# Kernel tuning notes

Measured on AMD Instinct MI355X. Metric: run time of the kernel, lower is better.

Reference implementation:

```python
import jax, jax.numpy as jnp
import numpy as np

ALPHA = 1.0
BETA = 0.25
NUM_EMBEDS = 8192
EMBED_DIM = 512
B, T = 32, 256


def setup_inputs() -> dict:
    key = jax.random.key(0)
    k1, k2 = jax.random.split(key)
    z_e = jax.random.normal(k1, (B, EMBED_DIM, T), dtype=jnp.float32)
    codebook = jax.random.normal(k2, (NUM_EMBEDS, EMBED_DIM), dtype=jnp.float32)
    return {"z_e": z_e, "codebook": codebook}


def reference(z_e, codebook):
    # z_e: (b, d, t) -> (b, t, d)
    z = jnp.transpose(z_e, (0, 2, 1))
    b, t, d = z.shape
    flat = z.reshape(-1, d)  # (N, d), N = b*t

    # squared euclidean distances to every codebook vector: (N, K)
    dists = (
        jnp.sum(flat * flat, axis=1, keepdims=True)
        + jnp.sum(codebook * codebook, axis=1)
        - 2.0 * flat @ codebook.T
    )
    idx = jnp.argmin(dists, axis=1)  # (N,)

    # codebook lookup (equivalent to one-hot @ codebook)
    z_q = codebook[idx].reshape(b, t, d)

    # commitment loss (codebook is EMA-updated, so only e_latent term)
    e_latent_loss = jnp.mean((jax.lax.stop_gradient(z_q) - z) ** 2)
    vq_loss = ALPHA * BETA * e_latent_loss

    # straight-through estimator
    z_q_st = z + jax.lax.stop_gradient(z_q - z)
    z_q_out = jnp.transpose(z_q_st, (0, 2, 1))  # back to (b, d, t)

    # perplexity from mean one-hot assignment probabilities
    counts = jnp.zeros((codebook.shape[0],), dtype=jnp.float32).at[idx].add(1.0)
    avg_probs = counts / flat.shape[0]
    perplexity = jnp.exp(-jnp.sum(avg_probs * jnp.log(avg_probs + 1e-10)))

    return z_q_out, vq_loss, perplexity
```

## Files before the change

### kernel.cpp

```cpp
#include <hip/hip_runtime.h>
#include <stdint.h>

typedef _Float16 half8 __attribute__((ext_vector_type(8)));
typedef float floatx16 __attribute__((ext_vector_type(16)));
typedef unsigned long long u64;

#define ALPHA_ 1.0f
#define BETA_ 0.25f
#define NUM_EMBEDS 8192
#define EMBED_DIM 512
#define B_ 32
#define T_ 256
#define N_TOK 8192
#define THR_GAP 2e-3f


typedef __attribute__((address_space(1))) const void ga_void;
typedef __attribute__((address_space(3))) void ls_void;
__device__ __forceinline__ void gl_lds16(const void* g, void* l) {
    __builtin_amdgcn_global_load_lds((ga_void*)g, (ls_void*)l, 16, 0, 0);
}

__device__ __forceinline__ uint32_t mono(float s) {
    uint32_t u = __float_as_uint(s);
    return (u & 0x80000000u) ? ~u : (u | 0x80000000u);
}
__device__ __forceinline__ float unmono(uint32_t v) {
    return __uint_as_float((v & 0x80000000u) ? (v ^ 0x80000000u) : ~v);
}

__global__ void pack_cb_kernel(const float* __restrict__ cb, _Float16* __restrict__ ci,
                               float* __restrict__ cnorm) {
    int row = blockIdx.x * 4 + (threadIdx.x >> 6);
    int lane = threadIdx.x & 63;
    const float* src = cb + (size_t)row * EMBED_DIM + lane * 8;
    float4 v0 = *(const float4*)src;
    float4 v1 = *(const float4*)(src + 4);
    float x[8] = {v0.x, v0.y, v0.z, v0.w, v1.x, v1.y, v1.z, v1.w};
    half8 hh, mm;
    float s = 0.f;
#pragma unroll
    for (int j = 0; j < 8; ++j) {
        s += x[j] * x[j];
        _Float16 hv = (_Float16)x[j];
        hh[j] = hv;
        mm[j] = (_Float16)((x[j] - (float)hv) * 2048.0f);
    }
    _Float16* dst = ci + (size_t)row * 1024 + lane * 16;
    *(half8*)dst = hh;
    *(half8*)(dst + 8) = mm;
#pragma unroll
    for (int d = 32; d; d >>= 1) s += __shfl_xor(s, d, 64);
    if (lane == 0) cnorm[row] = s;
}

__global__ void pack_z_kernel(const float* __restrict__ z, _Float16* __restrict__ zi) {
    int tid = threadIdx.x;
    int lane = tid & 63, ds = tid >> 6;
    int b = blockIdx.x >> 2;
    int t = ((blockIdx.x & 3) << 6) + lane;
    size_t n = (size_t)b * T_ + t;
    for (int g = 0; g < 16; ++g) {
        int d0 = g * 32 + ds * 8;
        const float* src = z + ((size_t)b * EMBED_DIM + d0) * T_ + t;
        half8 hh, mm;
#pragma unroll
        for (int j = 0; j < 8; ++j) {
            float x = -2.0f * src[(size_t)j * T_];
            _Float16 hv = (_Float16)x;
            hh[j] = hv;
            mm[j] = (_Float16)((x - (float)hv) * 2048.0f);
        }
        _Float16* dst = zi + n * 1024 + (size_t)(g * 4 + ds) * 16;
        *(half8*)dst = hh;
        *(half8*)(dst + 8) = mm;
    }
}

#define MFMA16(a, b, c) __builtin_amdgcn_mfma_f32_32x32x16_f16(a, b, c, 0, 0, 0)

__global__ __launch_bounds__(256, 2) void argmin_kernel(
    const _Float16* __restrict__ cb_i, const _Float16* __restrict__ zt_i,
    const float* __restrict__ cnorm, u64* __restrict__ slot_m1,
    _Float16* __restrict__ slot_d) {
    __shared__ _Float16 As[2][8192];
    __shared__ _Float16 Bs[2][8192];
    __shared__ u64 sK[128];
    __shared__ float sV1[128], sV2[128];
    const int tid = threadIdx.x;
    const int l = tid & 63;
    const int wv = tid >> 6;
    const int l31 = l & 31;
    const int hf = l >> 5;
    const int wp = wv >> 1, wq = wv & 1;
    const int n0 = blockIdx.x * 128;
    const int c0 = blockIdx.y * 128;

    const bool isA = wv < 2;
    const _Float16* gsrc = isA ? cb_i : zt_i;
    const int rbase = (isA ? c0 : n0) + ((wv & 1) << 6);
    const int srow = l >> 3;
    const int sseg = (l & 7) ^ srow;
    const size_t lanefix = (size_t)(rbase + srow) * 1024 + sseg * 8;

    floatx16 acc1[2][2], acc2[2][2];
#pragma unroll
    for (int a = 0; a < 2; ++a)
#pragma unroll
        for (int b = 0; b < 2; ++b)
#pragma unroll
            for (int r = 0; r < 16; ++r) { acc1[a][b][r] = 0.f; acc2[a][b][r] = 0.f; }

    auto stage = [&](int p, int s) {
        const _Float16* gs = gsrc + lanefix + (size_t)s * 64;
        _Float16* lb = (isA ? As[p] : Bs[p]) + ((wv & 1) << 12);
#pragma unroll
        for (int j = 0; j < 8; ++j)
            gl_lds16(gs + (size_t)j * 8192, lb + j * 512);
    };

    stage(0, 0);
    __syncthreads();
    for (int s = 0; s < 16; ++s) {
        const int p = s & 1;
        if (s < 15) stage(p ^ 1, s + 1);
        const _Float16* Ab = As[p] + (wp * 64 + l31) * 64;
        const _Float16* Bb = Bs[p] + (wq * 64 + l31) * 64;
        const int rs = l31 & 7;
#pragma unroll
        for (int kk = 0; kk < 2; ++kk) {
            const int j = kk * 2 + hf;
            const int ph = ((2 * j) ^ rs) * 8;
            const int pm = ((2 * j + 1) ^ rs) * 8;
            half8 Ah0 = *(const half8*)(Ab + ph), Am0 = *(const half8*)(Ab + pm);
            half8 Ah1 = *(const half8*)(Ab + 2048 + ph), Am1 = *(const half8*)(Ab + 2048 + pm);
            half8 Bh0 = *(const half8*)(Bb + ph), Bm0 = *(const half8*)(Bb + pm);
            half8 Bh1 = *(const half8*)(Bb + 2048 + ph), Bm1 = *(const half8*)(Bb + 2048 + pm);
            acc1[0][0] = MFMA16(Ah0, Bh0, acc1[0][0]);
            acc2[0][0] = MFMA16(Ah0, Bm0, acc2[0][0]);
            acc2[0][0] = MFMA16(Am0, Bh0, acc2[0][0]);
            acc1[0][1] = MFMA16(Ah0, Bh1, acc1[0][1]);
            acc2[0][1] = MFMA16(Ah0, Bm1, acc2[0][1]);
            acc2[0][1] = MFMA16(Am0, Bh1, acc2[0][1]);
            acc1[1][0] = MFMA16(Ah1, Bh0, acc1[1][0]);
            acc2[1][0] = MFMA16(Ah1, Bm0, acc2[1][0]);
            acc2[1][0] = MFMA16(Am1, Bh0, acc2[1][0]);
            acc1[1][1] = MFMA16(Ah1, Bh1, acc1[1][1]);
            acc2[1][1] = MFMA16(Ah1, Bm1, acc2[1][1]);
            acc2[1][1] = MFMA16(Am1, Bh1, acc2[1][1]);
        }
        __syncthreads();
    }

    u64 km[2]; float kv1[2], kv2[2];
#pragma unroll
    for (int qi = 0; qi < 2; ++qi) {
        u64 m1k = ~0ULL;
        float m1v = 3.4e38f, m2 = 3.4e38f;
#pragma unroll
        for (int ti = 0; ti < 2; ++ti)
#pragma unroll
            for (int g = 0; g < 4; ++g) {
                const int cb4 = c0 + wp * 64 + ti * 32 + g * 8 + hf * 4;
                float4 cn = *(const float4*)(cnorm + cb4);
                const floatx16& A1 = acc1[ti][qi];
                const floatx16& A2 = acc2[ti][qi];
                float sv[4] = {cn.x + A1[g * 4 + 0] + A2[g * 4 + 0] * (1.0f / 2048.0f),
                               cn.y + A1[g * 4 + 1] + A2[g * 4 + 1] * (1.0f / 2048.0f),
                               cn.z + A1[g * 4 + 2] + A2[g * 4 + 2] * (1.0f / 2048.0f),
                               cn.w + A1[g * 4 + 3] + A2[g * 4 + 3] * (1.0f / 2048.0f)};
#pragma unroll
                for (int q = 0; q < 4; ++q) {
                    u64 key = ((u64)mono(sv[q]) << 32) | (uint32_t)(cb4 + q);
                    if (key < m1k) { m2 = m1v; m1v = sv[q]; m1k = key; }
                    else m2 = fminf(m2, sv[q]);
                }
            }
        u64 ok = __shfl_xor(m1k, 32, 64);
        float ov = __shfl_xor(m1v, 32, 64);
        float om2 = __shfl_xor(m2, 32, 64);
        if (ok < m1k) { m2 = fminf(fminf(m2, om2), m1v); m1v = ov; m1k = ok; }
        else m2 = fminf(fminf(m2, om2), ov);
        km[qi] = m1k; kv1[qi] = m1v; kv2[qi] = m2;
    }
    if (wp == 1 && hf == 0) {
#pragma unroll
        for (int qi = 0; qi < 2; ++qi) {
            int idx = wq * 64 + qi * 32 + l31;
            sK[idx] = km[qi]; sV1[idx] = kv1[qi]; sV2[idx] = kv2[qi];
        }
    }
    __syncthreads();
    if (wp == 0 && hf == 0) {
#pragma unroll
        for (int qi = 0; qi < 2; ++qi) {
            int idx = wq * 64 + qi * 32 + l31;
            u64 m1k = km[qi]; float m1v = kv1[qi], m2 = kv2[qi];
            u64 ok = sK[idx]; float ov = sV1[idx], om2 = sV2[idx];
            if (ok < m1k) { m2 = fminf(fminf(m2, om2), m1v); m1v = ov; m1k = ok; }
            else m2 = fminf(fminf(m2, om2), ov);
            int tok = n0 + idx;
            slot_m1[((size_t)blockIdx.y << 13) + tok] = m1k;
            slot_d[((size_t)blockIdx.y << 13) + tok] = (_Float16)(m2 - m1v);
        }
    }
}

__global__ void combine_kernel(const u64* __restrict__ slot_m1, const _Float16* __restrict__ slot_d,
                               u64* __restrict__ wexact, int* __restrict__ worklist,
                               int* __restrict__ nflag) {
    int tok = blockIdx.x * 256 + threadIdx.x;
    u64 g1 = ~0ULL;
    float g1v = 3.4e38f, g2 = 3.4e38f;
    for (int c = 0; c < 64; ++c) {
        u64 k = slot_m1[((size_t)c << 13) + tok];
        float kv = unmono((uint32_t)(k >> 32));
        float v2 = kv + (float)slot_d[((size_t)c << 13) + tok];
        if (k < g1) { g2 = fminf(g2, g1v); g1 = k; g1v = kv; }
        else g2 = fminf(g2, kv);
        g2 = fminf(g2, v2);
    }
    if (g2 - g1v > THR_GAP) wexact[tok] = g1;
    else { int i = atomicAdd(nflag, 1); if (i < 8192) worklist[i] = tok; }
}

__global__ void fallback_kernel(const float* __restrict__ z, const float* __restrict__ cb,
                                const float* __restrict__ cnorm,
                                const int* __restrict__ worklist, const int* __restrict__ nflag,
                                u64* __restrict__ wexact) {
    int n = *nflag;
    if (n > 8192) n = 8192;
    const int l = threadIdx.x & 63, wv = threadIdx.x >> 6;
    const int cbase = blockIdx.x * 128;
    for (int fi = blockIdx.y; fi < n; fi += gridDim.y) {
        int tok = worklist[fi];
        int b = tok >> 8, t = tok & 255;
        const float* zp = z + ((size_t)b * EMBED_DIM) * T_ + t;
        float zr[8];
#pragma unroll
        for (int j = 0; j < 8; ++j) zr[j] = zp[(size_t)(l * 8 + j) * T_];
        u64 m1 = ~0ULL;
        for (int j = 0; j < 32; ++j) {
            int c = cbase + wv + j * 4;
            const float* cp = cb + (size_t)c * EMBED_DIM + l * 8;
            float4 a = *(const float4*)cp, bb = *(const float4*)(cp + 4);
            float dot = zr[0] * a.x + zr[1] * a.y + zr[2] * a.z + zr[3] * a.w +
                        zr[4] * bb.x + zr[5] * bb.y + zr[6] * bb.z + zr[7] * bb.w;
#pragma unroll
            for (int m = 32; m; m >>= 1) dot += __shfl_xor(dot, m, 64);
            if (l == 0) {
                float s = cnorm[c] - 2.0f * dot;
                u64 key = ((u64)mono(s) << 32) | (uint32_t)c;
                if (key < m1) m1 = key;
            }
        }
        if (l == 0) atomicMin(&wexact[tok], m1);
    }
}

__global__ void gather_kernel(const float* __restrict__ z, const float* __restrict__ cb,
                              const u64* __restrict__ wexact,
                              float* __restrict__ out, int* __restrict__ counts,
                              float* __restrict__ sse_acc) {
    __shared__ unsigned int sIdx[64];
    __shared__ float red[4];
    const int tid = threadIdx.x;
    const int n0 = blockIdx.x * 64;
    const int b = n0 >> 8;
    const int t0 = n0 & 255;
    if (tid < 64) {
        unsigned int idx = (unsigned int)(wexact[n0 + tid] & 0xffffffffULL);
        sIdx[tid] = idx;
        atomicAdd(&counts[idx], 1);
    }
    __syncthreads();
    const int w = tid >> 6;
    const int lane = tid & 63;
    const float* crow = cb + (size_t)sIdx[lane] * EMBED_DIM;
    const size_t base = ((size_t)b * EMBED_DIM) * T_ + (size_t)(t0 + lane);
    float sse = 0.f;
    for (int d = w; d < EMBED_DIM; d += 4) {
        float v = crow[d];
        size_t o = base + (size_t)d * T_;
        float diff = v - z[o];
        out[o] = v;
        sse += diff * diff;
    }
    for (int m = 32; m; m >>= 1) sse += __shfl_xor(sse, m, 64);
    if (lane == 0) red[w] = sse;
    __syncthreads();
    if (tid == 0) atomicAdd(sse_acc, red[0] + red[1] + red[2] + red[3]);
}

__global__ void finalize_kernel(const int* __restrict__ counts,
                                const float* __restrict__ sse_acc,
                                float* __restrict__ out) {
    __shared__ float red[4];
    const int tid = threadIdx.x;
    float e = 0.f;
    for (int k = tid; k < NUM_EMBEDS; k += 256) {
        float p = (float)counts[k] * (1.0f / (float)N_TOK);
        e += p * logf(p + 1e-10f);
    }
    for (int m = 32; m; m >>= 1) e += __shfl_xor(e, m, 64);
    if ((tid & 63) == 0) red[tid >> 6] = e;
    __syncthreads();
    if (tid == 0) {
        float ent = red[0] + red[1] + red[2] + red[3];
        size_t off = (size_t)B_ * EMBED_DIM * T_;
        out[off + 0] = (ALPHA_ * BETA_) * sse_acc[0] / (float)((size_t)N_TOK * EMBED_DIM);
        out[off + 1] = expf(-ent);
    }
}

extern "C" void kernel_launch(void* const* d_in, const int* in_sizes, int n_in,
                              void* d_out, int out_size, void* d_ws, size_t ws_size,
                              hipStream_t stream) {
    const float* z = (const float*)d_in[0];
    const float* cb = (const float*)d_in[1];
    float* out = (float*)d_out;
    char* ws = (char*)d_ws;
    u64* wexact = (u64*)ws;
    float* cnorm = (float*)(ws + 65536);
    int* counts = (int*)(ws + 98304);
    float* sse = (float*)(ws + 131072);
    int* nflag = (int*)(ws + 131076);
    int* worklist = (int*)(ws + 131080);
    u64* slot_m1 = (u64*)(ws + (1ull << 20));
    _Float16* slot_d = (_Float16*)(ws + (5ull << 20));
    _Float16* cb_i = (_Float16*)(ws + (6ull << 20));
    _Float16* zt_i = (_Float16*)(ws + (22ull << 20));

    hipMemsetAsync(wexact, 0xFF, NUM_EMBEDS * sizeof(u64), stream);
    hipMemsetAsync(counts, 0, NUM_EMBEDS * sizeof(int) + 8, stream);

    pack_cb_kernel<<<NUM_EMBEDS / 4, 256, 0, stream>>>(cb, cb_i, cnorm);
    pack_z_kernel<<<N_TOK / 64, 256, 0, stream>>>(z, zt_i);
    argmin_kernel<<<dim3(N_TOK / 128, NUM_EMBEDS / 128), 256, 0, stream>>>(cb_i, zt_i, cnorm, slot_m1, slot_d);
    combine_kernel<<<N_TOK / 256, 256, 0, stream>>>(slot_m1, slot_d, wexact, worklist, nflag);
    fallback_kernel<<<dim3(64, 16), 256, 0, stream>>>(z, cb, cnorm, worklist, nflag, wexact);
    gather_kernel<<<N_TOK / 64, 256, 0, stream>>>(z, cb, wexact, out, counts, sse);
    finalize_kernel<<<1, 256, 0, stream>>>(counts, sse, out);
}
```

Baseline: 363.3 us.

## Retile split-fp16 argmin GEMM, fuse pack/init kernels, pack slot data

The argmin GEMM now uses 256-token by 128-code tiles with a single combined accumulator per output tile instead of separate hi and correction accumulators. It also uses a K step of 32 over 32 stages and a new swizzled LDS layout, with the next stage's loads issued after the fragment reads. The two pack kernels and both memsets are merged into one launch. The per-slot min key and gap are packed into a single u64, so combine reads one array. The residual is stored unscaled, so its precision drops, and THR_GAP is raised to compensate, which may send more tokens to the exact fallback.

```diff
diff --git a/kernel.cpp b/kernel.cpp
--- a/kernel.cpp
+++ b/kernel.cpp
@@ -12,7 +12,7 @@
 #define B_ 32
 #define T_ 256
 #define N_TOK 8192
-#define THR_GAP 2e-3f
+#define THR_GAP 0.01f
 
 
 typedef __attribute__((address_space(1))) const void ga_void;
@@ -29,51 +29,62 @@
     return __uint_as_float((v & 0x80000000u) ? (v ^ 0x80000000u) : ~v);
 }
 
-__global__ void pack_cb_kernel(const float* __restrict__ cb, _Float16* __restrict__ ci,
-                               float* __restrict__ cnorm) {
-    int row = blockIdx.x * 4 + (threadIdx.x >> 6);
-    int lane = threadIdx.x & 63;
-    const float* src = cb + (size_t)row * EMBED_DIM + lane * 8;
-    float4 v0 = *(const float4*)src;
-    float4 v1 = *(const float4*)(src + 4);
-    float x[8] = {v0.x, v0.y, v0.z, v0.w, v1.x, v1.y, v1.z, v1.w};
-    half8 hh, mm;
-    float s = 0.f;
-#pragma unroll
-    for (int j = 0; j < 8; ++j) {
-        s += x[j] * x[j];
-        _Float16 hv = (_Float16)x[j];
-        hh[j] = hv;
-        mm[j] = (_Float16)((x[j] - (float)hv) * 2048.0f);
-    }
-    _Float16* dst = ci + (size_t)row * 1024 + lane * 16;
-    *(half8*)dst = hh;
-    *(half8*)(dst + 8) = mm;
-#pragma unroll
-    for (int d = 32; d; d >>= 1) s += __shfl_xor(s, d, 64);
-    if (lane == 0) cnorm[row] = s;
-}
-
-__global__ void pack_z_kernel(const float* __restrict__ z, _Float16* __restrict__ zi) {
-    int tid = threadIdx.x;
-    int lane = tid & 63, ds = tid >> 6;
-    int b = blockIdx.x >> 2;
-    int t = ((blockIdx.x & 3) << 6) + lane;
-    size_t n = (size_t)b * T_ + t;
-    for (int g = 0; g < 16; ++g) {
-        int d0 = g * 32 + ds * 8;
-        const float* src = z + ((size_t)b * EMBED_DIM + d0) * T_ + t;
+__global__ void pack_kernel(const float* __restrict__ cb, const float* __restrict__ z,
+                            _Float16* __restrict__ cb_i, _Float16* __restrict__ zt_i,
+                            float* __restrict__ cnorm, u64* __restrict__ wexact,
+                            int* __restrict__ counts, float* __restrict__ sse,
+                            int* __restrict__ nflag) {
+    const int bx = blockIdx.x;
+    const int tid = threadIdx.x;
+    if (bx < 2048) {
+        int row = bx * 4 + (tid >> 6);
+        int lane = tid & 63;
+        const float* src = cb + (size_t)row * EMBED_DIM + lane * 8;
+        float4 v0 = *(const float4*)src;
+        float4 v1 = *(const float4*)(src + 4);
+        float x[8] = {v0.x, v0.y, v0.z, v0.w, v1.x, v1.y, v1.z, v1.w};
         half8 hh, mm;
+        float s = 0.f;
 #pragma unroll
         for (int j = 0; j < 8; ++j) {
-            float x = -2.0f * src[(size_t)j * T_];
-            _Float16 hv = (_Float16)x;
+            s += x[j] * x[j];
+            _Float16 hv = (_Float16)x[j];
             hh[j] = hv;
-            mm[j] = (_Float16)((x - (float)hv) * 2048.0f);
-        }
-        _Float16* dst = zi + n * 1024 + (size_t)(g * 4 + ds) * 16;
+            mm[j] = (_Float16)(x[j] - (float)hv);
+        }
+        _Float16* dst = cb_i + (size_t)row * 1024 + (lane >> 1) * 32 + (lane & 1) * 8;
         *(half8*)dst = hh;
-        *(half8*)(dst + 8) = mm;
+        *(half8*)(dst + 16) = mm;
+#pragma unroll
+        for (int d = 32; d; d >>= 1) s += __shfl_xor(s, d, 64);
+        if (lane == 0) cnorm[row] = s;
+    } else if (bx < 2176) {
+        int bz = bx - 2048;
+        int lane = tid & 63, ds = tid >> 6;
+        int b = bz >> 2;
+        int t = ((bz & 3) << 6) + lane;
+        size_t n = (size_t)b * T_ + t;
+        for (int g = 0; g < 16; ++g) {
+            int d0 = g * 32 + ds * 8;
+            const float* src = z + ((size_t)b * EMBED_DIM + d0) * T_ + t;
+            half8 hh, mm;
+#pragma unroll
+            for (int j = 0; j < 8; ++j) {
+                float x = -2.0f * src[(size_t)j * T_];
+                _Float16 hv = (_Float16)x;
+                hh[j] = hv;
+                mm[j] = (_Float16)(x - (float)hv);
+            }
+            int gg = g * 4 + ds;
+            _Float16* dst = zt_i + n * 1024 + (gg >> 1) * 32 + (gg & 1) * 8;
+            *(half8*)dst = hh;
+            *(half8*)(dst + 16) = mm;
+        }
+    } else {
+        int i = bx - 2176;
+        wexact[i * 256 + tid] = ~0ULL;
+        counts[i * 256 + tid] = 0;
+        if (i == 0 && tid == 0) { *sse = 0.f; *nflag = 0; }
     }
 }
 
@@ -81,94 +92,113 @@
 
 __global__ __launch_bounds__(256, 2) void argmin_kernel(
     const _Float16* __restrict__ cb_i, const _Float16* __restrict__ zt_i,
-    const float* __restrict__ cnorm, u64* __restrict__ slot_m1,
-    _Float16* __restrict__ slot_d) {
-    __shared__ _Float16 As[2][8192];
-    __shared__ _Float16 Bs[2][8192];
-    __shared__ u64 sK[128];
-    __shared__ float sV1[128], sV2[128];
+    const float* __restrict__ cnorm, u64* __restrict__ slot) {
+    __shared__ _Float16 smem[24576];
+    __shared__ u64 sK[256];
+    __shared__ float sV1[256], sV2[256];
     const int tid = threadIdx.x;
     const int l = tid & 63;
     const int wv = tid >> 6;
     const int l31 = l & 31;
     const int hf = l >> 5;
     const int wp = wv >> 1, wq = wv & 1;
-    const int n0 = blockIdx.x * 128;
+    const int n0 = blockIdx.x * 256;
     const int c0 = blockIdx.y * 128;
 
-    const bool isA = wv < 2;
-    const _Float16* gsrc = isA ? cb_i : zt_i;
-    const int rbase = (isA ? c0 : n0) + ((wv & 1) << 6);
-    const int srow = l >> 3;
-    const int sseg = (l & 7) ^ srow;
-    const size_t lanefix = (size_t)(rbase + srow) * 1024 + sseg * 8;
-
-    floatx16 acc1[2][2], acc2[2][2];
-#pragma unroll
-    for (int a = 0; a < 2; ++a)
-#pragma unroll
-        for (int b = 0; b < 2; ++b)
-#pragma unroll
-            for (int r = 0; r < 16; ++r) { acc1[a][b][r] = 0.f; acc2[a][b][r] = 0.f; }
-
-    auto stage = [&](int p, int s) {
-        const _Float16* gs = gsrc + lanefix + (size_t)s * 64;
-        _Float16* lb = (isA ? As[p] : Bs[p]) + ((wv & 1) << 12);
-#pragma unroll
-        for (int j = 0; j < 8; ++j)
-            gl_lds16(gs + (size_t)j * 8192, lb + j * 512);
+    const _Float16* gptr[6];
+    int lofs[6], bmul[6];
+#pragma unroll
+    for (int j = 0; j < 6; ++j) {
+        int id = wv * 6 + j;
+        if (id < 8) {
+            int rp = id * 4 + (l >> 4);
+            int lid = (l & 15) ^ (rp & 15);
+            gptr[j] = cb_i + (size_t)(c0 + (lid >> 2) * 32 + rp) * 1024 + (lid & 3) * 8;
+            lofs[j] = id * 512 + l * 8;
+            bmul[j] = 4096;
+        } else {
+            int bid = id - 8;
+            int rp = bid * 4 + (l >> 4);
+            int lid = (l & 15) ^ (rp & 15);
+            gptr[j] = zt_i + (size_t)(n0 + (lid >> 2) * 64 + rp) * 1024 + (lid & 3) * 8;
+            lofs[j] = 8192 + bid * 512 + l * 8;
+            bmul[j] = 8192;
+        }
+    }
+    auto stagefull = [&](int buf, int ss) {
+        const int ga = ss * 32;
+#pragma unroll
+        for (int j = 0; j < 6; ++j)
+            gl_lds16(gptr[j] + ga, smem + lofs[j] + buf * bmul[j]);
     };
 
-    stage(0, 0);
-    __syncthreads();
-    for (int s = 0; s < 16; ++s) {
-        const int p = s & 1;
-        if (s < 15) stage(p ^ 1, s + 1);
-        const _Float16* Ab = As[p] + (wp * 64 + l31) * 64;
-        const _Float16* Bb = Bs[p] + (wq * 64 + l31) * 64;
-        const int rs = l31 & 7;
-#pragma unroll
-        for (int kk = 0; kk < 2; ++kk) {
-            const int j = kk * 2 + hf;
-            const int ph = ((2 * j) ^ rs) * 8;
-            const int pm = ((2 * j + 1) ^ rs) * 8;
-            half8 Ah0 = *(const half8*)(Ab + ph), Am0 = *(const half8*)(Ab + pm);
-            half8 Ah1 = *(const half8*)(Ab + 2048 + ph), Am1 = *(const half8*)(Ab + 2048 + pm);
-            half8 Bh0 = *(const half8*)(Bb + ph), Bm0 = *(const half8*)(Bb + pm);
-            half8 Bh1 = *(const half8*)(Bb + 2048 + ph), Bm1 = *(const half8*)(Bb + 2048 + pm);
-            acc1[0][0] = MFMA16(Ah0, Bh0, acc1[0][0]);
-            acc2[0][0] = MFMA16(Ah0, Bm0, acc2[0][0]);
-            acc2[0][0] = MFMA16(Am0, Bh0, acc2[0][0]);
-            acc1[0][1] = MFMA16(Ah0, Bh1, acc1[0][1]);
-            acc2[0][1] = MFMA16(Ah0, Bm1, acc2[0][1]);
-            acc2[0][1] = MFMA16(Am0, Bh1, acc2[0][1]);
-            acc1[1][0] = MFMA16(Ah1, Bh0, acc1[1][0]);
-            acc2[1][0] = MFMA16(Ah1, Bm0, acc2[1][0]);
-            acc2[1][0] = MFMA16(Am1, Bh0, acc2[1][0]);
-            acc1[1][1] = MFMA16(Ah1, Bh1, acc1[1][1]);
-            acc2[1][1] = MFMA16(Ah1, Bm1, acc2[1][1]);
-            acc2[1][1] = MFMA16(Am1, Bh1, acc2[1][1]);
-        }
+    int aoff[2][2], boff[4][2];
+#pragma unroll
+    for (int pi = 0; pi < 2; ++pi)
+#pragma unroll
+        for (int p = 0; p < 2; ++p) {
+            int lid = (wp * 2 + pi) * 4 + p * 2 + hf;
+            aoff[pi][p] = l31 * 128 + (lid ^ (l31 & 15)) * 8;
+        }
+#pragma unroll
+    for (int qi = 0; qi < 4; ++qi)
+#pragma unroll
+        for (int p = 0; p < 2; ++p) {
+            int lid = (wq * 2 + (qi >> 1)) * 4 + p * 2 + hf;
+            boff[qi][p] = 8192 + ((qi & 1) * 32 + l31) * 128 + (lid ^ (l31 & 15)) * 8;
+        }
+
+    floatx16 acc[2][4];
+#pragma unroll
+    for (int pi = 0; pi < 2; ++pi)
+#pragma unroll
+        for (int qi = 0; qi < 4; ++qi)
+#pragma unroll
+            for (int r = 0; r < 16; ++r) acc[pi][qi][r] = 0.f;
+
+    stagefull(0, 0);
+    __syncthreads();
+    for (int ss = 0; ss < 32; ++ss) {
+        const int buf = ss & 1;
+        const int ab = buf * 4096, bb = buf * 8192;
+        half8 Ah[2], Am[2], Bh[4], Bm[4];
+#pragma unroll
+        for (int pi = 0; pi < 2; ++pi) {
+            Ah[pi] = *(const half8*)(smem + aoff[pi][0] + ab);
+            Am[pi] = *(const half8*)(smem + aoff[pi][1] + ab);
+        }
+#pragma unroll
+        for (int qi = 0; qi < 4; ++qi) {
+            Bh[qi] = *(const half8*)(smem + boff[qi][0] + bb);
+            Bm[qi] = *(const half8*)(smem + boff[qi][1] + bb);
+        }
+        if (ss < 31) stagefull(buf ^ 1, ss + 1);
+#pragma unroll
+        for (int pi = 0; pi < 2; ++pi)
+#pragma unroll
+            for (int qi = 0; qi < 4; ++qi) {
+                acc[pi][qi] = MFMA16(Ah[pi], Bh[qi], acc[pi][qi]);
+                acc[pi][qi] = MFMA16(Am[pi], Bh[qi], acc[pi][qi]);
+                acc[pi][qi] = MFMA16(Ah[pi], Bm[qi], acc[pi][qi]);
+            }
         __syncthreads();
     }
 
-    u64 km[2]; float kv1[2], kv2[2];
-#pragma unroll
-    for (int qi = 0; qi < 2; ++qi) {
+    u64 qk[4];
+    float qv1[4], qv2[4];
+#pragma unroll
+    for (int qi = 0; qi < 4; ++qi) {
         u64 m1k = ~0ULL;
         float m1v = 3.4e38f, m2 = 3.4e38f;
 #pragma unroll
-        for (int ti = 0; ti < 2; ++ti)
+        for (int pi = 0; pi < 2; ++pi)
 #pragma unroll
             for (int g = 0; g < 4; ++g) {
-                const int cb4 = c0 + wp * 64 + ti * 32 + g * 8 + hf * 4;
+                const int cb4 = c0 + wp * 64 + pi * 32 + g * 8 + hf * 4;
                 float4 cn = *(const float4*)(cnorm + cb4);
-                const floatx16& A1 = acc1[ti][qi];
-                const floatx16& A2 = acc2[ti][qi];
-                float sv[4] = {cn.x + A1[g * 4 + 0] + A2[g * 4 + 0] * (1.0f / 2048.0f),
-                               cn.y + A1[g * 4 + 1] + A2[g * 4 + 1] * (1.0f / 2048.0f),
-                               cn.z + A1[g * 4 + 2] + A2[g * 4 + 2] * (1.0f / 2048.0f),
-                               cn.w + A1[g * 4 + 3] + A2[g * 4 + 3] * (1.0f / 2048.0f)};
+                const floatx16& A = acc[pi][qi];
+                float sv[4] = {cn.x + A[g * 4 + 0], cn.y + A[g * 4 + 1],
+                               cn.z + A[g * 4 + 2], cn.w + A[g * 4 + 3]};
 #pragma unroll
                 for (int q = 0; q < 4; ++q) {
                     u64 key = ((u64)mono(sv[q]) << 32) | (uint32_t)(cb4 + q);
@@ -181,46 +211,47 @@
         float om2 = __shfl_xor(m2, 32, 64);
         if (ok < m1k) { m2 = fminf(fminf(m2, om2), m1v); m1v = ov; m1k = ok; }
         else m2 = fminf(fminf(m2, om2), ov);
-        km[qi] = m1k; kv1[qi] = m1v; kv2[qi] = m2;
+        qk[qi] = m1k; qv1[qi] = m1v; qv2[qi] = m2;
     }
     if (wp == 1 && hf == 0) {
 #pragma unroll
-        for (int qi = 0; qi < 2; ++qi) {
-            int idx = wq * 64 + qi * 32 + l31;
-            sK[idx] = km[qi]; sV1[idx] = kv1[qi]; sV2[idx] = kv2[qi];
+        for (int qi = 0; qi < 4; ++qi) {
+            const int tl = wq * 128 + qi * 32 + l31;
+            sK[tl] = qk[qi]; sV1[tl] = qv1[qi]; sV2[tl] = qv2[qi];
         }
     }
     __syncthreads();
     if (wp == 0 && hf == 0) {
 #pragma unroll
-        for (int qi = 0; qi < 2; ++qi) {
-            int idx = wq * 64 + qi * 32 + l31;
-            u64 m1k = km[qi]; float m1v = kv1[qi], m2 = kv2[qi];
-            u64 ok = sK[idx]; float ov = sV1[idx], om2 = sV2[idx];
+        for (int qi = 0; qi < 4; ++qi) {
+            const int tl = wq * 128 + qi * 32 + l31;
+            u64 m1k = qk[qi]; float m1v = qv1[qi], m2 = qv2[qi];
+            u64 ok = sK[tl]; float ov = sV1[tl], om2 = sV2[tl];
             if (ok < m1k) { m2 = fminf(fminf(m2, om2), m1v); m1v = ov; m1k = ok; }
             else m2 = fminf(fminf(m2, om2), ov);
-            int tok = n0 + idx;
-            slot_m1[((size_t)blockIdx.y << 13) + tok] = m1k;
-            slot_d[((size_t)blockIdx.y << 13) + tok] = (_Float16)(m2 - m1v);
-        }
-    }
-}
-
-__global__ void combine_kernel(const u64* __restrict__ slot_m1, const _Float16* __restrict__ slot_d,
-                               u64* __restrict__ wexact, int* __restrict__ worklist,
-                               int* __restrict__ nflag) {
+            uint32_t code = (uint32_t)m1k & 0x1FFFu;
+            uint32_t d16 = (uint32_t)__builtin_bit_cast(unsigned short, (_Float16)(m2 - m1v));
+            slot[((size_t)blockIdx.y << 13) + n0 + tl] =
+                (m1k & 0xFFFFFFFF00000000ULL) | ((u64)code << 16) | d16;
+        }
+    }
+}
+
+__global__ void combine_kernel(const u64* __restrict__ slot, u64* __restrict__ wexact,
+                               int* __restrict__ worklist, int* __restrict__ nflag) {
     int tok = blockIdx.x * 256 + threadIdx.x;
     u64 g1 = ~0ULL;
     float g1v = 3.4e38f, g2 = 3.4e38f;
     for (int c = 0; c < 64; ++c) {
-        u64 k = slot_m1[((size_t)c << 13) + tok];
-        float kv = unmono((uint32_t)(k >> 32));
-        float v2 = kv + (float)slot_d[((size_t)c << 13) + tok];
-        if (k < g1) { g2 = fminf(g2, g1v); g1 = k; g1v = kv; }
+        u64 v = slot[((size_t)c << 13) + tok];
+        float kv = unmono((uint32_t)(v >> 32));
+        float d = (float)__builtin_bit_cast(_Float16, (unsigned short)(v & 0xffff));
+        if (v < g1) { g2 = fminf(g2, g1v); g1 = v; g1v = kv; }
         else g2 = fminf(g2, kv);
-        g2 = fminf(g2, v2);
-    }
-    if (g2 - g1v > THR_GAP) wexact[tok] = g1;
+        g2 = fminf(g2, kv + d);
+    }
+    if (g2 - g1v > THR_GAP)
+        wexact[tok] = (g1 & 0xFFFFFFFF00000000ULL) | ((g1 >> 16) & 0x1FFFULL);
     else { int i = atomicAdd(nflag, 1); if (i < 8192) worklist[i] = tok; }
 }
 
@@ -269,7 +300,7 @@
     const int b = n0 >> 8;
     const int t0 = n0 & 255;
     if (tid < 64) {
-        unsigned int idx = (unsigned int)(wexact[n0 + tid] & 0xffffffffULL);
+        unsigned int idx = (unsigned int)(wexact[n0 + tid] & 0x1FFFULL);
         sIdx[tid] = idx;
         atomicAdd(&counts[idx], 1);
     }
@@ -326,18 +357,13 @@
     float* sse = (float*)(ws + 131072);
     int* nflag = (int*)(ws + 131076);
     int* worklist = (int*)(ws + 131080);
-    u64* slot_m1 = (u64*)(ws + (1ull << 20));
-    _Float16* slot_d = (_Float16*)(ws + (5ull << 20));
+    u64* slot = (u64*)(ws + (1ull << 20));
     _Float16* cb_i = (_Float16*)(ws + (6ull << 20));
     _Float16* zt_i = (_Float16*)(ws + (22ull << 20));
 
-    hipMemsetAsync(wexact, 0xFF, NUM_EMBEDS * sizeof(u64), stream);
-    hipMemsetAsync(counts, 0, NUM_EMBEDS * sizeof(int) + 8, stream);
-
-    pack_cb_kernel<<<NUM_EMBEDS / 4, 256, 0, stream>>>(cb, cb_i, cnorm);
-    pack_z_kernel<<<N_TOK / 64, 256, 0, stream>>>(z, zt_i);
-    argmin_kernel<<<dim3(N_TOK / 128, NUM_EMBEDS / 128), 256, 0, stream>>>(cb_i, zt_i, cnorm, slot_m1, slot_d);
-    combine_kernel<<<N_TOK / 256, 256, 0, stream>>>(slot_m1, slot_d, wexact, worklist, nflag);
+    pack_kernel<<<2208, 256, 0, stream>>>(cb, z, cb_i, zt_i, cnorm, wexact, counts, sse, nflag);
+    argmin_kernel<<<dim3(N_TOK / 256, NUM_EMBEDS / 128), 256, 0, stream>>>(cb_i, zt_i, cnorm, slot);
+    combine_kernel<<<N_TOK / 256, 256, 0, stream>>>(slot, wexact, worklist, nflag);
     fallback_kernel<<<dim3(64, 16), 256, 0, stream>>>(z, cb, cnorm, worklist, nflag, wexact);
     gather_kernel<<<N_TOK / 64, 256, 0, stream>>>(z, cb, wexact, out, counts, sse);
     finalize_kernel<<<1, 256, 0, stream>>>(counts, sse, out);
```

After: 378.6 us. 1.04x slower.
